# Optimization experiments

Hardware: AMD Instinct MI355X
Metric: run time of the kernel (lower is better)

Reference implementation:

```python
import jax, jax.numpy as jnp
import numpy as np

H, DH, ITERS, EPS, LN_EPS = 8, 32, 3, 1e-8, 1e-5

def _ln(x, w, b):
    m = jnp.mean(x, axis=-1, keepdims=True)
    v = jnp.mean(jnp.square(x - m), axis=-1, keepdims=True)
    return (x - m) * jax.lax.rsqrt(v + LN_EPS) * w + b

def setup_inputs() -> dict:
    key = jax.random.key(0)
    ks = jax.random.split(key, 16)
    B, N, D, S = 64, 4096, 256, 8
    DI = H * DH  # 256
    HID = max(D, 128)
    s = 0.02
    return {
        "inputs": jax.random.normal(ks[0], (B, N, D), jnp.float32),
        "noise": jax.random.normal(ks[1], (B, S, D), jnp.float32),
        "slots_mean": jax.random.normal(ks[2], (1, 1, D), jnp.float32),
        "slots_logvar": jax.random.normal(ks[3], (1, 1, D), jnp.float32) * s,
        "wq": jax.random.normal(ks[4], (D, DI), jnp.float32) * s,
        "bq": jnp.zeros((DI,), jnp.float32),
        "wk": jax.random.normal(ks[5], (D, DI), jnp.float32) * s,
        "bk": jnp.zeros((DI,), jnp.float32),
        "wv": jax.random.normal(ks[6], (D, DI), jnp.float32) * s,
        "bv": jnp.zeros((DI,), jnp.float32),
        "wo": jax.random.normal(ks[7], (DI, D), jnp.float32) * s,
        "bo": jnp.zeros((D,), jnp.float32),
        "w_ih": jax.random.normal(ks[8], (D, 3 * D), jnp.float32) * s,
        "b_ih": jnp.zeros((3 * D,), jnp.float32),
        "w_hh": jax.random.normal(ks[9], (D, 3 * D), jnp.float32) * s,
        "b_hh": jnp.zeros((3 * D,), jnp.float32),
        "w1": jax.random.normal(ks[10], (D, HID), jnp.float32) * s,
        "b1": jnp.zeros((HID,), jnp.float32),
        "w2": jax.random.normal(ks[11], (HID, D), jnp.float32) * s,
        "b2": jnp.zeros((D,), jnp.float32),
        "ln_in_w": jnp.ones((D,), jnp.float32), "ln_in_b": jnp.zeros((D,), jnp.float32),
        "ln_s_w": jnp.ones((D,), jnp.float32), "ln_s_b": jnp.zeros((D,), jnp.float32),
        "ln_ff_w": jnp.ones((D,), jnp.float32), "ln_ff_b": jnp.zeros((D,), jnp.float32),
    }

def reference(inputs, noise, slots_mean, slots_logvar, wq, bq, wk, bk, wv, bv,
              wo, bo, w_ih, b_ih, w_hh, b_hh, w1, b1, w2, b2,
              ln_in_w, ln_in_b, ln_s_w, ln_s_b, ln_ff_w, ln_ff_b):
    B, N, D = inputs.shape
    S = noise.shape[1]
    scale = D ** -0.5  # note: scale uses dim, per original code
    # slot init: mean + exp(logvar) * noise (faithful: exp(logvar) used directly)
    slots = slots_mean + jnp.exp(slots_logvar) * noise  # [B,S,D]
    x = _ln(inputs, ln_in_w, ln_in_b)
    k = (x @ wk + bk).reshape(B, N, H, DH).transpose(0, 2, 1, 3)  # [B,H,N,Dh]
    v = (x @ wv + bv).reshape(B, N, H, DH).transpose(0, 2, 1, 3)
    attn = None
    for _ in range(ITERS):
        slots_prev = slots
        s = _ln(slots, ln_s_w, ln_s_b)
        q = (s @ wq + bq).reshape(B, S, H, DH).transpose(0, 2, 1, 3)  # [B,H,S,Dh]
        dots = jnp.einsum('bhid,bhjd->bhij', q, k) * scale  # [B,H,S,N]
        attn = jax.nn.softmax(dots, axis=-2)  # softmax over slot axis
        attn = attn + EPS
        attn = attn / jnp.clip(jnp.sum(attn, axis=-1, keepdims=True), 1e-12)  # L1 over inputs
        upd = jnp.einsum('bhjd,bhij->bhid', v, attn)  # [B,H,S,Dh]
        upd = upd.transpose(0, 2, 1, 3).reshape(B, S, H * DH) @ wo + bo  # [B,S,D]
        # GRUCell (torch gate order r,z,n)
        xg = upd.reshape(B * S, D) @ w_ih + b_ih
        hg = slots_prev.reshape(B * S, D) @ w_hh + b_hh
        xr, xz, xn = jnp.split(xg, 3, axis=-1)
        hr, hz, hn = jnp.split(hg, 3, axis=-1)
        r = jax.nn.sigmoid(xr + hr)
        z = jax.nn.sigmoid(xz + hz)
        n = jnp.tanh(xn + r * hn)
        slots = ((1.0 - z) * n + z * slots_prev.reshape(B * S, D)).reshape(B, S, D)
        ff = _ln(slots, ln_ff_w, ln_ff_b)
        slots = slots + (jax.nn.relu(ff @ w1 + b1) @ w2 + b2)
    return slots, attn
```

## Files before the change

kernel.cpp:

```cpp
#include <hip/hip_runtime.h>
#include <stdint.h>

typedef __attribute__((ext_vector_type(8))) short bf16x8;
typedef __attribute__((ext_vector_type(4))) float f32x4;

__device__ __forceinline__ float b2f(unsigned short s) {
    unsigned int u = ((unsigned int)s) << 16;
    return __builtin_bit_cast(float, u);
}
__device__ __forceinline__ unsigned short f2b(float f) {
    unsigned int u = __builtin_bit_cast(unsigned int, f);
    u += 0x7FFFu + ((u >> 16) & 1u);
    return (unsigned short)(u >> 16);
}

#define EPS_ATTN 1e-8f
#define LN_EPS 1e-5f
#define SCALE 0.0625f

__global__ __launch_bounds__(256) void k_prep(const float* __restrict__ wk,
                                              const float* __restrict__ wv,
                                              unsigned short* __restrict__ W3) {
    int g = blockIdx.x * 256 + threadIdx.x;
    int j = g & 7;
    int f = (g >> 3) & 1023;
    int stage = g >> 13;
    int p = f & 15, qq = (f >> 4) & 3, ntl = f >> 6;
    int kc = stage >> 1, half_ = stage & 1;
    int k = kc * 32 + qq * 8 + j;
    int n = half_ * 256 + ntl * 16 + p;
    float v = (n < 256) ? wk[k * 256 + n] : wv[k * 256 + (n - 256)];
    W3[g] = f2b(v);
}

__global__ __launch_bounds__(256) void k_init(const float* __restrict__ sm,
                                              const float* __restrict__ slv,
                                              const float* __restrict__ noise,
                                              float* __restrict__ slots) {
    int idx = blockIdx.x * 256 + threadIdx.x;
    int d = idx & 255;
    slots[idx] = sm[d] + expf(slv[d]) * noise[idx];
}

__global__ __launch_bounds__(256, 2) void k_kv(
    const float* __restrict__ x, const float* __restrict__ lnw, const float* __restrict__ lnb,
    const unsigned short* __restrict__ W3, const float* __restrict__ bk, const float* __restrict__ bv,
    unsigned short* __restrict__ Kb, unsigned short* __restrict__ Vb) {
    __shared__ __align__(16) unsigned short sh[16384];
    __shared__ __align__(16) float bL[512];
    unsigned short* As = sh;
    int t = threadIdx.x;
    int w = t >> 6, lane = t & 63;
    int p = lane & 15, q = lane >> 4;

    if (t < 128) {
        float4 bb = (t < 64) ? ((const float4*)bk)[t] : ((const float4*)bv)[t - 64];
        *(float4*)&bL[t * 4] = bb;
    }

    float4 lw  = ((const float4*)lnw)[lane];
    float4 lbv = ((const float4*)lnb)[lane];
    float4 xv[16];
    const float* xbase = x + ((size_t)blockIdx.x * 64 + w * 16) * 256;
    #pragma unroll
    for (int i = 0; i < 16; ++i) xv[i] = ((const float4*)(xbase + i * 256))[lane];
    int kcw = lane >> 3, qw = (lane >> 1) & 3, j0 = (lane & 1) * 4;
    #pragma unroll
    for (int i = 0; i < 16; ++i) {
        float4 v = xv[i];
        float s0 = v.x + v.y + v.z + v.w;
        float s1 = v.x * v.x + v.y * v.y + v.z * v.z + v.w * v.w;
        #pragma unroll
        for (int o = 1; o < 64; o <<= 1) { s0 += __shfl_xor(s0, o); s1 += __shfl_xor(s1, o); }
        float mean = s0 * (1.0f / 256.0f);
        float var  = s1 * (1.0f / 256.0f) - mean * mean;
        float rstd = rsqrtf(var + LN_EPS);
        ushort4 pk;
        pk.x = f2b((v.x - mean) * rstd * lw.x + lbv.x);
        pk.y = f2b((v.y - mean) * rstd * lw.y + lbv.y);
        pk.z = f2b((v.z - mean) * rstd * lw.z + lbv.z);
        pk.w = f2b((v.w - mean) * rstd * lw.w + lbv.w);
        int pos = (qw * 16 + i) ^ kcw;
        *(ushort4*)&As[((w * 8 + kcw) * 64 + pos) * 8 + j0] = pk;
    }
    __syncthreads();

    f32x4 acc[4][8];
    f32x4 zero = {0.f, 0.f, 0.f, 0.f};
    #pragma unroll
    for (int rt = 0; rt < 4; ++rt)
        #pragma unroll
        for (int ct = 0; ct < 8; ++ct) acc[rt][ct] = zero;

    const unsigned short* Wb = W3 + (size_t)(w >> 1) * 8192 + (size_t)((w & 1) * 8) * 512 + lane * 8;
    #pragma unroll 2
    for (int kc = 0; kc < 8; ++kc) {
        bf16x8 af[4];
        #pragma unroll
        for (int rt = 0; rt < 4; ++rt)
            af[rt] = *(const bf16x8*)&As[((rt * 8 + kc) * 64 + ((q * 16 + p) ^ kc)) * 8];
        #pragma unroll
        for (int ct = 0; ct < 8; ++ct) {
            bf16x8 bf = *(const bf16x8*)(Wb + (size_t)kc * 16384 + ct * 512);
            #pragma unroll
            for (int rt = 0; rt < 4; ++rt)
                acc[rt][ct] = __builtin_amdgcn_mfma_f32_16x16x32_bf16(af[rt], bf, acc[rt][ct], 0, 0, 0);
        }
    }
    __syncthreads();

    unsigned short* rep = As;
    int b_  = blockIdx.x >> 6;
    int n0g = (blockIdx.x & 63) * 64;

    if (w < 2) {
        #pragma unroll
        for (int ct = 0; ct < 8; ++ct) {
            int col = w * 128 + ct * 16 + p;
            float bias = bL[col];
            int hl = col >> 5, dh = col & 31;
            #pragma unroll
            for (int rt = 0; rt < 4; ++rt) {
                #pragma unroll
                for (int r = 0; r < 4; ++r) {
                    int nl = rt * 16 + q * 4 + r;
                    rep[(hl * 64 + nl) * 32 + dh] = f2b(acc[rt][ct][r] + bias);
                }
            }
        }
    }
    __syncthreads();
    #pragma unroll
    for (int i = 0; i < 8; ++i) {
        uint4 vd = *(const uint4*)&rep[(i * 256 + t) * 8];
        *(uint4*)(Kb + (((size_t)b_ * 8 + i) * 4096 + n0g) * 32 + t * 8) = vd;
    }
    __syncthreads();

    if (w >= 2) {
        #pragma unroll
        for (int ct = 0; ct < 8; ++ct) {
            int vrow = (w - 2) * 128 + ct * 16 + p;
            float bias = bL[256 + vrow];
            #pragma unroll
            for (int rt = 0; rt < 4; ++rt) {
                int chunk = (rt * 4 + q) ^ (p & 14);
                ushort4 pk;
                pk.x = f2b(acc[rt][ct][0] + bias);
                pk.y = f2b(acc[rt][ct][1] + bias);
                pk.z = f2b(acc[rt][ct][2] + bias);
                pk.w = f2b(acc[rt][ct][3] + bias);
                *(ushort4*)&rep[vrow * 64 + chunk * 4] = pk;
            }
        }
    }
    __syncthreads();
    #pragma unroll
    for (int i = 0; i < 8; ++i) {
        int vrow = i * 32 + (t >> 3);
        int c16 = t & 7;
        uint4 vd = *(const uint4*)&rep[vrow * 64 + ((2 * c16) ^ (vrow & 14)) * 4];
        *(uint4*)(Vb + ((size_t)(b_ * 8 + (vrow >> 5)) * 32 + (vrow & 31)) * 4096 + n0g + c16 * 8) = vd;
    }
}

__global__ __launch_bounds__(256) void k_q(
    const float* __restrict__ slots, const float* __restrict__ lnw, const float* __restrict__ lnb,
    const float* __restrict__ wq, const float* __restrict__ bq, float* __restrict__ qg) {
    __shared__ float sln[256];
    __shared__ float red[8];
    int t = threadIdx.x;
    int row = blockIdx.x;
    float v = slots[(size_t)row * 256 + t];
    float s0 = v, s1 = v * v;
    #pragma unroll
    for (int off = 1; off < 64; off <<= 1) { s0 += __shfl_xor(s0, off); s1 += __shfl_xor(s1, off); }
    if ((t & 63) == 0) { red[t >> 6] = s0; red[4 + (t >> 6)] = s1; }
    __syncthreads();
    float ts0 = red[0] + red[1] + red[2] + red[3];
    float ts1 = red[4] + red[5] + red[6] + red[7];
    float mean = ts0 * (1.f / 256.f);
    float var  = ts1 * (1.f / 256.f) - mean * mean;
    float rstd = rsqrtf(var + LN_EPS);
    sln[t] = (v - mean) * rstd * lnw[t] + lnb[t];
    __syncthreads();
    float acc = bq[t];
    #pragma unroll 4
    for (int k = 0; k < 256; ++k) acc += sln[k] * wq[k * 256 + t];
    int b = row >> 3, sl = row & 7;
    qg[(size_t)b * 2048 + (t >> 5) * 256 + sl * 32 + (t & 31)] = acc;
}

__global__ __launch_bounds__(256) void k_attn(
    const unsigned short* __restrict__ Kg, const unsigned short* __restrict__ VTg,
    const float* __restrict__ qg, float* __restrict__ upd_part, float* __restrict__ rowsum_part,
    float* __restrict__ attn_out, int last) {
    __shared__ float supd[4][256];
    __shared__ float srs[4][8];
    int t = threadIdx.x;
    int w = t >> 6, lane = t & 63;
    int c = lane & 15;
    int g = lane >> 4;

    int bh = blockIdx.x >> 2;
    int chunk = blockIdx.x & 3;
    const unsigned short* Kbh = Kg  + (size_t)bh * 4096 * 32;
    const unsigned short* Vbh = VTg + (size_t)bh * 32 * 4096;

    bf16x8 qhi = {0,0,0,0,0,0,0,0};
    bf16x8 qlo = {0,0,0,0,0,0,0,0};
    if (c < 8) {
        const float* qp = qg + (size_t)bh * 256 + c * 32 + g * 8;
        #pragma unroll
        for (int j = 0; j < 8; ++j) {
            float qv = qp[j];
            unsigned short hb = f2b(qv);
            qhi[j] = (short)hb;
            qlo[j] = (short)f2b(qv - b2f(hb));
        }
    }

    f32x4 zero = {0.f, 0.f, 0.f, 0.f};
    f32x4 accL = zero, accH = zero;
    float rs = 0.f;
    int nb0 = chunk * 1024 + w * 256;

    #pragma unroll 2
    for (int pr = 0; pr < 8; ++pr) {
        int base = nb0 + pr * 32;
        bf16x8 k0 = *(const bf16x8*)(Kbh + (size_t)(base + c) * 32 + g * 8);
        bf16x8 k1 = *(const bf16x8*)(Kbh + (size_t)(base + 16 + c) * 32 + g * 8);
        const unsigned short* vlo = Vbh + (size_t)c * 4096 + base + g * 4;
        const unsigned short* vhi = Vbh + (size_t)(c + 16) * 4096 + base + g * 4;
        union { ushort4 h[2]; bf16x8 v; } V0, V1;
        V0.h[0] = *(const ushort4*)vlo;
        V0.h[1] = *(const ushort4*)(vlo + 16);
        V1.h[0] = *(const ushort4*)vhi;
        V1.h[1] = *(const ushort4*)(vhi + 16);

        f32x4 s0 = __builtin_amdgcn_mfma_f32_16x16x32_bf16(k0, qhi, zero, 0, 0, 0);
        s0 = __builtin_amdgcn_mfma_f32_16x16x32_bf16(k0, qlo, s0, 0, 0, 0);
        f32x4 s1 = __builtin_amdgcn_mfma_f32_16x16x32_bf16(k1, qhi, zero, 0, 0, 0);
        s1 = __builtin_amdgcn_mfma_f32_16x16x32_bf16(k1, qlo, s1, 0, 0, 0);

        float d0[4], d1[4];
        #pragma unroll
        for (int r = 0; r < 4; ++r) { d0[r] = s0[r] * SCALE; d1[r] = s1[r] * SCALE; }
        float m = fmaxf(fmaxf(fmaxf(d0[0], d0[1]), fmaxf(d0[2], d0[3])),
                        fmaxf(fmaxf(d1[0], d1[1]), fmaxf(d1[2], d1[3])));
        m = fmaxf(m, __shfl_xor(m, 1));
        m = fmaxf(m, __shfl_xor(m, 2));
        m = fmaxf(m, __shfl_xor(m, 4));
        m = fmaxf(m, __shfl_xor(m, 8));
        float a0[4], a1[4];
        #pragma unroll
        for (int r = 0; r < 4; ++r) {
            float e0 = __expf(d0[r] - m);
            float e1 = __expf(d1[r] - m);
            float t0 = e0;
            t0 += __shfl_xor(t0, 1); t0 += __shfl_xor(t0, 2); t0 += __shfl_xor(t0, 4);
            float t1 = e1;
            t1 += __shfl_xor(t1, 1); t1 += __shfl_xor(t1, 2); t1 += __shfl_xor(t1, 4);
            a0[r] = e0 * (1.0f / t0) + EPS_ATTN;
            a1[r] = e1 * (1.0f / t1) + EPS_ATTN;
            rs += a0[r] + a1[r];
        }
        if (last && c < 8) {
            float4 st0 = {a0[0], a0[1], a0[2], a0[3]};
            float4 st1 = {a1[0], a1[1], a1[2], a1[3]};
            float* ap = attn_out + ((size_t)bh * 8 + c) * 4096 + base + g * 4;
            *(float4*)ap = st0;
            *(float4*)(ap + 16) = st1;
        }
        bf16x8 pah, pal;
        float af[8] = {a0[0], a0[1], a0[2], a0[3], a1[0], a1[1], a1[2], a1[3]};
        #pragma unroll
        for (int j = 0; j < 8; ++j) {
            unsigned short hb = f2b(af[j]);
            pah[j] = (short)hb;
            pal[j] = (short)f2b(af[j] - b2f(hb));
        }
        accL = __builtin_amdgcn_mfma_f32_16x16x32_bf16(V0.v, pah, accL, 0, 0, 0);
        accL = __builtin_amdgcn_mfma_f32_16x16x32_bf16(V0.v, pal, accL, 0, 0, 0);
        accH = __builtin_amdgcn_mfma_f32_16x16x32_bf16(V1.v, pah, accH, 0, 0, 0);
        accH = __builtin_amdgcn_mfma_f32_16x16x32_bf16(V1.v, pal, accH, 0, 0, 0);
    }

    rs += __shfl_xor(rs, 16);
    rs += __shfl_xor(rs, 32);
    if (lane < 8) srs[w][lane] = rs;
    if (c < 8) {
        float* up = &supd[w][c * 32 + g * 4];
        up[0]  = accL[0]; up[1]  = accL[1]; up[2]  = accL[2]; up[3]  = accL[3];
        up[16] = accH[0]; up[17] = accH[1]; up[18] = accH[2]; up[19] = accH[3];
    }
    __syncthreads();
    {
        float v = supd[0][t] + supd[1][t] + supd[2][t] + supd[3][t];
        upd_part[((size_t)bh * 4 + chunk) * 256 + t] = v;
    }
    if (t < 8) {
        float v = srs[0][t] + srs[1][t] + srs[2][t] + srs[3][t];
        rowsum_part[((size_t)bh * 4 + chunk) * 8 + t] = v;
    }
}

__global__ __launch_bounds__(256) void k_gA(
    const float* __restrict__ upd_part, const float* __restrict__ rowsum_part,
    const float* __restrict__ wo, const float* __restrict__ bo,
    float* __restrict__ O, float* __restrict__ rowsum_tot) {
    __shared__ float Ul[8][256];
    __shared__ float Pp[4][8][64];
    int t = threadIdx.x;
    int b = blockIdx.x >> 2, cc = blockIdx.x & 3;
    int colbase = cc * 64;
    {
        int r = t >> 5, d0 = (t & 31) * 8;
        int h = (t & 31) >> 2;
        float rsum = 0.f;
        #pragma unroll
        for (int ch = 0; ch < 4; ++ch)
            rsum += rowsum_part[((size_t)(b * 8 + h) * 4 + ch) * 8 + r];
        float inv = 1.0f / fmaxf(rsum, 1e-12f);
        float u[8] = {0.f,0.f,0.f,0.f,0.f,0.f,0.f,0.f};
        #pragma unroll
        for (int ch = 0; ch < 4; ++ch) {
            const float* up = upd_part + ((size_t)(b * 8 + h) * 4 + ch) * 256 + r * 32 + (d0 & 31);
            float4 u0 = *(const float4*)up;
            float4 u1 = *(const float4*)(up + 4);
            u[0] += u0.x; u[1] += u0.y; u[2] += u0.z; u[3] += u0.w;
            u[4] += u1.x; u[5] += u1.y; u[6] += u1.z; u[7] += u1.w;
        }
        #pragma unroll
        for (int i = 0; i < 8; ++i) Ul[r][d0 + i] = u[i] * inv;
        if (cc == 0 && (t & 3) == 0) rowsum_tot[(b * 8 + h) * 8 + r] = rsum;
    }
    __syncthreads();
    int c = t & 63, kq = t >> 6;
    float acc[8] = {0.f,0.f,0.f,0.f,0.f,0.f,0.f,0.f};
    const float* wp = wo + (size_t)(kq * 64) * 256 + colbase + c;
    #pragma unroll 16
    for (int k = 0; k < 64; ++k) {
        float wv_ = wp[(size_t)k * 256];
        int kk = kq * 64 + k;
        #pragma unroll
        for (int r = 0; r < 8; ++r) acc[r] += Ul[r][kk] * wv_;
    }
    #pragma unroll
    for (int r = 0; r < 8; ++r) Pp[kq][r][c] = acc[r];
    __syncthreads();
    #pragma unroll
    for (int j = 0; j < 2; ++j) {
        int o = t * 2 + j;
        int r = o >> 6, c2 = o & 63;
        float v = Pp[0][r][c2] + Pp[1][r][c2] + Pp[2][r][c2] + Pp[3][r][c2] + bo[colbase + c2];
        O[(size_t)(b * 8 + r) * 256 + colbase + c2] = v;
    }
}

__global__ __launch_bounds__(256) void k_gB(
    const float* __restrict__ O, const float* __restrict__ slin,
    const float* __restrict__ wih, const float* __restrict__ bih,
    const float* __restrict__ whh, const float* __restrict__ bhh,
    float* __restrict__ gcomb, float* __restrict__ xn, float* __restrict__ hn) {
    __shared__ float Ol[8][256], Hl[8][256];
    __shared__ float Px[2][8][128], Ph[2][8][128];
    int t = threadIdx.x;
    int b = blockIdx.x / 6, cc = blockIdx.x % 6;
    int colbase = cc * 128;
    {
        int r = t >> 5, d0 = (t & 31) * 8;
        const float* op = O + (size_t)(b * 8 + r) * 256 + d0;
        const float* hp = slin + (size_t)(b * 8 + r) * 256 + d0;
        *(float4*)&Ol[r][d0]     = *(const float4*)op;
        *(float4*)&Ol[r][d0 + 4] = *(const float4*)(op + 4);
        *(float4*)&Hl[r][d0]     = *(const float4*)hp;
        *(float4*)&Hl[r][d0 + 4] = *(const float4*)(hp + 4);
    }
    __syncthreads();
    int c = t & 127, kh = t >> 7;
    float ax[8] = {0.f,0.f,0.f,0.f,0.f,0.f,0.f,0.f};
    float ah[8] = {0.f,0.f,0.f,0.f,0.f,0.f,0.f,0.f};
    const float* wxp = wih + (size_t)(kh * 128) * 768 + colbase + c;
    const float* whp = whh + (size_t)(kh * 128) * 768 + colbase + c;
    #pragma unroll 8
    for (int k = 0; k < 128; ++k) {
        float wx = wxp[(size_t)k * 768];
        float wh = whp[(size_t)k * 768];
        int kk = kh * 128 + k;
        #pragma unroll
        for (int r = 0; r < 8; ++r) { ax[r] += Ol[r][kk] * wx; ah[r] += Hl[r][kk] * wh; }
    }
    #pragma unroll
    for (int r = 0; r < 8; ++r) { Px[kh][r][c] = ax[r]; Ph[kh][r][c] = ah[r]; }
    __syncthreads();
    #pragma unroll
    for (int j = 0; j < 4; ++j) {
        int o = t * 4 + j;
        int r = o >> 7, c2 = o & 127;
        int cg = colbase + c2;
        int row = b * 8 + r;
        float vx = Px[0][r][c2] + Px[1][r][c2] + bih[cg];
        float vh = Ph[0][r][c2] + Ph[1][r][c2] + bhh[cg];
        if (cg < 512) {
            gcomb[(size_t)row * 512 + cg] = vx + vh;
        } else {
            xn[(size_t)row * 256 + cg - 512] = vx;
            hn[(size_t)row * 256 + cg - 512] = vh;
        }
    }
}

__global__ __launch_bounds__(256) void k_gC(
    const float* __restrict__ gcomb, const float* __restrict__ xn, const float* __restrict__ hn,
    const float* __restrict__ slin, const float* __restrict__ lnfw, const float* __restrict__ lnfb,
    float* __restrict__ slout, float* __restrict__ F) {
    __shared__ float red[8];
    int t = threadIdx.x, row = blockIdx.x;
    float a_r = gcomb[(size_t)row * 512 + t];
    float a_z = gcomb[(size_t)row * 512 + 256 + t];
    float xnv = xn[(size_t)row * 256 + t];
    float hnv = hn[(size_t)row * 256 + t];
    float hp  = slin[(size_t)row * 256 + t];
    float rg = 1.f / (1.f + expf(-a_r));
    float zg = 1.f / (1.f + expf(-a_z));
    float ng = tanhf(xnv + rg * hnv);
    float s1 = (1.f - zg) * ng + zg * hp;
    slout[(size_t)row * 256 + t] = s1;
    float s0 = s1, sq = s1 * s1;
    #pragma unroll
    for (int o = 1; o < 64; o <<= 1) { s0 += __shfl_xor(s0, o); sq += __shfl_xor(sq, o); }
    if ((t & 63) == 0) { red[t >> 6] = s0; red[4 + (t >> 6)] = sq; }
    __syncthreads();
    float ts0 = red[0] + red[1] + red[2] + red[3];
    float ts1 = red[4] + red[5] + red[6] + red[7];
    float mean = ts0 * (1.f / 256.f);
    float var  = ts1 * (1.f / 256.f) - mean * mean;
    float rstd = rsqrtf(var + LN_EPS);
    F[(size_t)row * 256 + t] = (s1 - mean) * rstd * lnfw[t] + lnfb[t];
}

__global__ __launch_bounds__(256) void k_gD(
    const float* __restrict__ F, const float* __restrict__ w1, const float* __restrict__ b1,
    float* __restrict__ H1) {
    __shared__ float Fl[8][256];
    __shared__ float Pp[4][8][64];
    int t = threadIdx.x;
    int b = blockIdx.x >> 2, cc = blockIdx.x & 3;
    int colbase = cc * 64;
    {
        int r = t >> 5, d0 = (t & 31) * 8;
        const float* fp = F + (size_t)(b * 8 + r) * 256 + d0;
        *(float4*)&Fl[r][d0]     = *(const float4*)fp;
        *(float4*)&Fl[r][d0 + 4] = *(const float4*)(fp + 4);
    }
    __syncthreads();
    int c = t & 63, kq = t >> 6;
    float acc[8] = {0.f,0.f,0.f,0.f,0.f,0.f,0.f,0.f};
    const float* wp = w1 + (size_t)(kq * 64) * 256 + colbase + c;
    #pragma unroll 16
    for (int k = 0; k < 64; ++k) {
        float wv_ = wp[(size_t)k * 256];
        int kk = kq * 64 + k;
        #pragma unroll
        for (int r = 0; r < 8; ++r) acc[r] += Fl[r][kk] * wv_;
    }
    #pragma unroll
    for (int r = 0; r < 8; ++r) Pp[kq][r][c] = acc[r];
    __syncthreads();
    #pragma unroll
    for (int j = 0; j < 2; ++j) {
        int o = t * 2 + j;
        int r = o >> 6, c2 = o & 63;
        float v = Pp[0][r][c2] + Pp[1][r][c2] + Pp[2][r][c2] + Pp[3][r][c2] + b1[colbase + c2];
        H1[(size_t)(b * 8 + r) * 256 + colbase + c2] = fmaxf(v, 0.f);
    }
}

__global__ __launch_bounds__(256) void k_gE(
    const float* __restrict__ H1, const float* __restrict__ w2, const float* __restrict__ b2,
    float* __restrict__ slout) {
    __shared__ float Hl[8][256];
    __shared__ float Pp[4][8][64];
    int t = threadIdx.x;
    int b = blockIdx.x >> 2, cc = blockIdx.x & 3;
    int colbase = cc * 64;
    {
        int r = t >> 5, d0 = (t & 31) * 8;
        const float* hp = H1 + (size_t)(b * 8 + r) * 256 + d0;
        *(float4*)&Hl[r][d0]     = *(const float4*)hp;
        *(float4*)&Hl[r][d0 + 4] = *(const float4*)(hp + 4);
    }
    __syncthreads();
    int c = t & 63, kq = t >> 6;
    float acc[8] = {0.f,0.f,0.f,0.f,0.f,0.f,0.f,0.f};
    const float* wp = w2 + (size_t)(kq * 64) * 256 + colbase + c;
    #pragma unroll 16
    for (int k = 0; k < 64; ++k) {
        float wv_ = wp[(size_t)k * 256];
        int kk = kq * 64 + k;
        #pragma unroll
        for (int r = 0; r < 8; ++r) acc[r] += Hl[r][kk] * wv_;
    }
    #pragma unroll
    for (int r = 0; r < 8; ++r) Pp[kq][r][c] = acc[r];
    __syncthreads();
    #pragma unroll
    for (int j = 0; j < 2; ++j) {
        int o = t * 2 + j;
        int r = o >> 6, c2 = o & 63;
        size_t idx = (size_t)(b * 8 + r) * 256 + colbase + c2;
        float v = Pp[0][r][c2] + Pp[1][r][c2] + Pp[2][r][c2] + Pp[3][r][c2] + b2[colbase + c2];
        slout[idx] = slout[idx] + v;
    }
}

__global__ __launch_bounds__(256) void k_scale(float* __restrict__ attn, const float* __restrict__ rowsum_tot) {
    size_t i4 = ((size_t)blockIdx.x * 256 + threadIdx.x) * 4;
    int row = (int)(i4 >> 12);
    float inv = 1.0f / fmaxf(rowsum_tot[row], 1e-12f);
    float4 v = *(float4*)(attn + i4);
    v.x *= inv; v.y *= inv; v.z *= inv; v.w *= inv;
    *(float4*)(attn + i4) = v;
}

extern "C" void kernel_launch(void* const* d_in, const int* in_sizes, int n_in,
                              void* d_out, int out_size, void* d_ws, size_t ws_size,
                              hipStream_t stream) {
    const float* inputs = (const float*)d_in[0];
    const float* noise  = (const float*)d_in[1];
    const float* sm     = (const float*)d_in[2];
    const float* slv    = (const float*)d_in[3];
    const float* wq     = (const float*)d_in[4];
    const float* bq     = (const float*)d_in[5];
    const float* wk     = (const float*)d_in[6];
    const float* bk     = (const float*)d_in[7];
    const float* wv     = (const float*)d_in[8];
    const float* bv     = (const float*)d_in[9];
    const float* wo     = (const float*)d_in[10];
    const float* bo     = (const float*)d_in[11];
    const float* wih    = (const float*)d_in[12];
    const float* bih    = (const float*)d_in[13];
    const float* whh    = (const float*)d_in[14];
    const float* bhh    = (const float*)d_in[15];
    const float* w1     = (const float*)d_in[16];
    const float* b1     = (const float*)d_in[17];
    const float* w2     = (const float*)d_in[18];
    const float* b2     = (const float*)d_in[19];
    const float* lniw   = (const float*)d_in[20];
    const float* lnib   = (const float*)d_in[21];
    const float* lnsw   = (const float*)d_in[22];
    const float* lnsb   = (const float*)d_in[23];
    const float* lnfw   = (const float*)d_in[24];
    const float* lnfb   = (const float*)d_in[25];

    char* ws = (char*)d_ws;
    unsigned short* Kb = (unsigned short*)ws;
    unsigned short* Vb = (unsigned short*)(ws + 134217728ull);
    float* slotsA  = (float*)(ws + 268435456ull);
    float* slotsB  = (float*)(ws + 268959744ull);
    float* Rr      = (float*)(ws + 269484032ull);
    float* Pr      = (float*)(ws + 270008320ull);
    float* Qr      = (float*)(ws + 270532608ull);
    float* rowsum_part = (float*)(ws + 272629760ull);
    float* rowsum_tot  = (float*)(ws + 273154048ull);
    unsigned short* W3 = (unsigned short*)Pr;
    float* O_  = Pr;
    float* upd_part = Qr;
    float* gcomb = Qr;
    float* xn = Qr + 262144;
    float* hn = Qr + 393216;
    float* H1 = Qr;
    float* qg = Rr;
    float* F_ = Rr;

    float* out_slots = (float*)d_out;
    float* attn_out  = (float*)d_out + 131072;

    k_prep<<<512, 256, 0, stream>>>(wk, wv, W3);
    k_init<<<512, 256, 0, stream>>>(sm, slv, noise, slotsA);
    k_kv<<<4096, 256, 0, stream>>>(inputs, lniw, lnib, W3, bk, bv, Kb, Vb);
    for (int it = 0; it < 3; ++it) {
        int last = (it == 2);
        float* sl_in  = (it == 0) ? slotsA : ((it == 1) ? slotsB : slotsA);
        float* sl_out = (it == 0) ? slotsB : ((it == 1) ? slotsA : out_slots);
        k_q<<<512, 256, 0, stream>>>(sl_in, lnsw, lnsb, wq, bq, qg);
        k_attn<<<2048, 256, 0, stream>>>(Kb, Vb, qg, upd_part, rowsum_part, attn_out, last);
        k_gA<<<256, 256, 0, stream>>>(upd_part, rowsum_part, wo, bo, O_, rowsum_tot);
        k_gB<<<384, 256, 0, stream>>>(O_, sl_in, wih, bih, whh, bhh, gcomb, xn, hn);
        k_gC<<<512, 256, 0, stream>>>(gcomb, xn, hn, sl_in, lnfw, lnfb, sl_out, F_);
        k_gD<<<256, 256, 0, stream>>>(F_, w1, b1, H1);
        k_gE<<<256, 256, 0, stream>>>(H1, w2, b2, sl_out);
    }
    k_scale<<<16384, 256, 0, stream>>>(attn_out, rowsum_tot);
}
```

Before: 1.098 ms.

## Precompute last-iteration attention rowsums to fold normalization into attn store; rebalance k_kv epilogue

On the last iteration a new k_pre kernel recomputes the softmax row sums from K and q, so k_attn can write attention already L1-normalized. This removes the separate k_scale pass that re-read and re-wrote the 64 MB fp32 attention output. It costs an extra read of K and a second QK^T/softmax pass. Separately, k_kv now gives every wave a share of both K and V columns and swizzles the K staging in LDS, so all four waves take part in each epilogue phase instead of two sitting idle.

New measurement: 1.025 ms. 1.07x faster.

```diff
diff --git a/kernel.cpp b/kernel.cpp
--- a/kernel.cpp
+++ b/kernel.cpp
@@ -92,7 +92,7 @@
         #pragma unroll
         for (int ct = 0; ct < 8; ++ct) acc[rt][ct] = zero;
 
-    const unsigned short* Wb = W3 + (size_t)(w >> 1) * 8192 + (size_t)((w & 1) * 8) * 512 + lane * 8;
+    const unsigned short* WbL = W3 + lane * 8;
     #pragma unroll 2
     for (int kc = 0; kc < 8; ++kc) {
         bf16x8 af[4];
@@ -101,7 +101,9 @@
             af[rt] = *(const bf16x8*)&As[((rt * 8 + kc) * 64 + ((q * 16 + p) ^ kc)) * 8];
         #pragma unroll
         for (int ct = 0; ct < 8; ++ct) {
-            bf16x8 bf = *(const bf16x8*)(Wb + (size_t)kc * 16384 + ct * 512);
+            int half_ = ct >> 2;
+            int ntl = w * 4 + (ct & 3);
+            bf16x8 bf = *(const bf16x8*)(WbL + (size_t)kc * 16384 + half_ * 8192 + ntl * 512);
             #pragma unroll
             for (int rt = 0; rt < 4; ++rt)
                 acc[rt][ct] = __builtin_amdgcn_mfma_f32_16x16x32_bf16(af[rt], bf, acc[rt][ct], 0, 0, 0);
@@ -113,45 +115,47 @@
     int b_  = blockIdx.x >> 6;
     int n0g = (blockIdx.x & 63) * 64;
 
-    if (w < 2) {
-        #pragma unroll
-        for (int ct = 0; ct < 8; ++ct) {
-            int col = w * 128 + ct * 16 + p;
-            float bias = bL[col];
-            int hl = col >> 5, dh = col & 31;
+    #pragma unroll
+    for (int ct = 0; ct < 4; ++ct) {
+        int col = w * 64 + ct * 16 + p;
+        float bias = bL[col];
+        int hl = col >> 5, dh = col & 31;
+        int dlo = dh & 7, dch = dh >> 3;
+        int dchs = dch ^ q;
+        #pragma unroll
+        for (int rt = 0; rt < 4; ++rt) {
             #pragma unroll
-            for (int rt = 0; rt < 4; ++rt) {
-                #pragma unroll
-                for (int r = 0; r < 4; ++r) {
-                    int nl = rt * 16 + q * 4 + r;
-                    rep[(hl * 64 + nl) * 32 + dh] = f2b(acc[rt][ct][r] + bias);
-                }
+            for (int r = 0; r < 4; ++r) {
+                int nl = rt * 16 + q * 4 + r;
+                rep[(hl * 64 + nl) * 32 + dchs * 8 + dlo] = f2b(acc[rt][ct][r] + bias);
             }
         }
     }
     __syncthreads();
-    #pragma unroll
-    for (int i = 0; i < 8; ++i) {
-        uint4 vd = *(const uint4*)&rep[(i * 256 + t) * 8];
-        *(uint4*)(Kb + (((size_t)b_ * 8 + i) * 4096 + n0g) * 32 + t * 8) = vd;
-    }
-    __syncthreads();
-
-    if (w >= 2) {
-        #pragma unroll
-        for (int ct = 0; ct < 8; ++ct) {
-            int vrow = (w - 2) * 128 + ct * 16 + p;
-            float bias = bL[256 + vrow];
-            #pragma unroll
-            for (int rt = 0; rt < 4; ++rt) {
-                int chunk = (rt * 4 + q) ^ (p & 14);
-                ushort4 pk;
-                pk.x = f2b(acc[rt][ct][0] + bias);
-                pk.y = f2b(acc[rt][ct][1] + bias);
-                pk.z = f2b(acc[rt][ct][2] + bias);
-                pk.w = f2b(acc[rt][ct][3] + bias);
-                *(ushort4*)&rep[vrow * 64 + chunk * 4] = pk;
-            }
+    {
+        int nl = t >> 2, dhc = t & 3;
+        int swz = (nl >> 2) & 3;
+        #pragma unroll
+        for (int i = 0; i < 8; ++i) {
+            uint4 vd = *(const uint4*)&rep[((i * 64 + nl) * 32) + ((dhc ^ swz) * 8)];
+            *(uint4*)(Kb + (((size_t)b_ * 8 + i) * 4096 + n0g + nl) * 32 + dhc * 8) = vd;
+        }
+    }
+    __syncthreads();
+
+    #pragma unroll
+    for (int ct = 4; ct < 8; ++ct) {
+        int vrow = w * 64 + (ct - 4) * 16 + p;
+        float bias = bL[256 + vrow];
+        #pragma unroll
+        for (int rt = 0; rt < 4; ++rt) {
+            int chunk = (rt * 4 + q) ^ (p & 14);
+            ushort4 pk;
+            pk.x = f2b(acc[rt][ct][0] + bias);
+            pk.y = f2b(acc[rt][ct][1] + bias);
+            pk.z = f2b(acc[rt][ct][2] + bias);
+            pk.w = f2b(acc[rt][ct][3] + bias);
+            *(ushort4*)&rep[vrow * 64 + chunk * 4] = pk;
         }
     }
     __syncthreads();
@@ -191,6 +195,73 @@
     qg[(size_t)b * 2048 + (t >> 5) * 256 + sl * 32 + (t & 31)] = acc;
 }
 
+__global__ __launch_bounds__(256) void k_pre(
+    const unsigned short* __restrict__ Kg, const float* __restrict__ qg,
+    float* __restrict__ rowsum_part) {
+    __shared__ float srs[4][8];
+    int t = threadIdx.x;
+    int w = t >> 6, lane = t & 63;
+    int c = lane & 15, g = lane >> 4;
+    int bh = blockIdx.x >> 2;
+    int chunk = blockIdx.x & 3;
+    const unsigned short* Kbh = Kg + (size_t)bh * 4096 * 32;
+
+    bf16x8 qhi = {0,0,0,0,0,0,0,0};
+    bf16x8 qlo = {0,0,0,0,0,0,0,0};
+    if (c < 8) {
+        const float* qp = qg + (size_t)bh * 256 + c * 32 + g * 8;
+        #pragma unroll
+        for (int j = 0; j < 8; ++j) {
+            float qv = qp[j];
+            unsigned short hb = f2b(qv);
+            qhi[j] = (short)hb;
+            qlo[j] = (short)f2b(qv - b2f(hb));
+        }
+    }
+
+    f32x4 zero = {0.f, 0.f, 0.f, 0.f};
+    float rs = 0.f;
+    int nb0 = chunk * 1024 + w * 256;
+
+    #pragma unroll 2
+    for (int pr = 0; pr < 8; ++pr) {
+        int base = nb0 + pr * 32;
+        bf16x8 k0 = *(const bf16x8*)(Kbh + (size_t)(base + c) * 32 + g * 8);
+        bf16x8 k1 = *(const bf16x8*)(Kbh + (size_t)(base + 16 + c) * 32 + g * 8);
+        f32x4 s0 = __builtin_amdgcn_mfma_f32_16x16x32_bf16(k0, qhi, zero, 0, 0, 0);
+        s0 = __builtin_amdgcn_mfma_f32_16x16x32_bf16(k0, qlo, s0, 0, 0, 0);
+        f32x4 s1 = __builtin_amdgcn_mfma_f32_16x16x32_bf16(k1, qhi, zero, 0, 0, 0);
+        s1 = __builtin_amdgcn_mfma_f32_16x16x32_bf16(k1, qlo, s1, 0, 0, 0);
+        float d0[4], d1[4];
+        #pragma unroll
+        for (int r = 0; r < 4; ++r) { d0[r] = s0[r] * SCALE; d1[r] = s1[r] * SCALE; }
+        float m = fmaxf(fmaxf(fmaxf(d0[0], d0[1]), fmaxf(d0[2], d0[3])),
+                        fmaxf(fmaxf(d1[0], d1[1]), fmaxf(d1[2], d1[3])));
+        m = fmaxf(m, __shfl_xor(m, 1));
+        m = fmaxf(m, __shfl_xor(m, 2));
+        m = fmaxf(m, __shfl_xor(m, 4));
+        m = fmaxf(m, __shfl_xor(m, 8));
+        #pragma unroll
+        for (int r = 0; r < 4; ++r) {
+            float e0 = __expf(d0[r] - m);
+            float e1 = __expf(d1[r] - m);
+            float t0 = e0;
+            t0 += __shfl_xor(t0, 1); t0 += __shfl_xor(t0, 2); t0 += __shfl_xor(t0, 4);
+            float t1 = e1;
+            t1 += __shfl_xor(t1, 1); t1 += __shfl_xor(t1, 2); t1 += __shfl_xor(t1, 4);
+            rs += (e0 * (1.0f / t0) + EPS_ATTN) + (e1 * (1.0f / t1) + EPS_ATTN);
+        }
+    }
+    rs += __shfl_xor(rs, 16);
+    rs += __shfl_xor(rs, 32);
+    if (lane < 8) srs[w][lane] = rs;
+    __syncthreads();
+    if (t < 8) {
+        rowsum_part[((size_t)bh * 4 + chunk) * 8 + t] =
+            srs[0][t] + srs[1][t] + srs[2][t] + srs[3][t];
+    }
+}
+
 __global__ __launch_bounds__(256) void k_attn(
     const unsigned short* __restrict__ Kg, const unsigned short* __restrict__ VTg,
     const float* __restrict__ qg, float* __restrict__ upd_part, float* __restrict__ rowsum_part,
@@ -218,6 +289,13 @@
             qhi[j] = (short)hb;
             qlo[j] = (short)f2b(qv - b2f(hb));
         }
+    }
+    float ainv = 0.f;
+    if (last && c < 8) {
+        float rsum = 0.f;
+        #pragma unroll
+        for (int ch = 0; ch < 4; ++ch) rsum += rowsum_part[((size_t)bh * 4 + ch) * 8 + c];
+        ainv = 1.0f / fmaxf(rsum, 1e-12f);
     }
 
     f32x4 zero = {0.f, 0.f, 0.f, 0.f};
@@ -266,8 +344,8 @@
             rs += a0[r] + a1[r];
         }
         if (last && c < 8) {
-            float4 st0 = {a0[0], a0[1], a0[2], a0[3]};
-            float4 st1 = {a1[0], a1[1], a1[2], a1[3]};
+            float4 st0 = {a0[0] * ainv, a0[1] * ainv, a0[2] * ainv, a0[3] * ainv};
+            float4 st1 = {a1[0] * ainv, a1[1] * ainv, a1[2] * ainv, a1[3] * ainv};
             float* ap = attn_out + ((size_t)bh * 8 + c) * 4096 + base + g * 4;
             *(float4*)ap = st0;
             *(float4*)(ap + 16) = st1;
@@ -286,9 +364,11 @@
         accH = __builtin_amdgcn_mfma_f32_16x16x32_bf16(V1.v, pal, accH, 0, 0, 0);
     }
 
-    rs += __shfl_xor(rs, 16);
-    rs += __shfl_xor(rs, 32);
-    if (lane < 8) srs[w][lane] = rs;
+    if (!last) {
+        rs += __shfl_xor(rs, 16);
+        rs += __shfl_xor(rs, 32);
+        if (lane < 8) srs[w][lane] = rs;
+    }
     if (c < 8) {
         float* up = &supd[w][c * 32 + g * 4];
         up[0]  = accL[0]; up[1]  = accL[1]; up[2]  = accL[2]; up[3]  = accL[3];
@@ -299,7 +379,7 @@
         float v = supd[0][t] + supd[1][t] + supd[2][t] + supd[3][t];
         upd_part[((size_t)bh * 4 + chunk) * 256 + t] = v;
     }
-    if (t < 8) {
+    if (!last && t < 8) {
         float v = srs[0][t] + srs[1][t] + srs[2][t] + srs[3][t];
         rowsum_part[((size_t)bh * 4 + chunk) * 8 + t] = v;
     }
@@ -308,7 +388,7 @@
 __global__ __launch_bounds__(256) void k_gA(
     const float* __restrict__ upd_part, const float* __restrict__ rowsum_part,
     const float* __restrict__ wo, const float* __restrict__ bo,
-    float* __restrict__ O, float* __restrict__ rowsum_tot) {
+    float* __restrict__ O) {
     __shared__ float Ul[8][256];
     __shared__ float Pp[4][8][64];
     int t = threadIdx.x;
@@ -333,7 +413,6 @@
         }
         #pragma unroll
         for (int i = 0; i < 8; ++i) Ul[r][d0 + i] = u[i] * inv;
-        if (cc == 0 && (t & 3) == 0) rowsum_tot[(b * 8 + h) * 8 + r] = rsum;
     }
     __syncthreads();
     int c = t & 63, kq = t >> 6;
@@ -513,15 +592,6 @@
         float v = Pp[0][r][c2] + Pp[1][r][c2] + Pp[2][r][c2] + Pp[3][r][c2] + b2[colbase + c2];
         slout[idx] = slout[idx] + v;
     }
-}
-
-__global__ __launch_bounds__(256) void k_scale(float* __restrict__ attn, const float* __restrict__ rowsum_tot) {
-    size_t i4 = ((size_t)blockIdx.x * 256 + threadIdx.x) * 4;
-    int row = (int)(i4 >> 12);
-    float inv = 1.0f / fmaxf(rowsum_tot[row], 1e-12f);
-    float4 v = *(float4*)(attn + i4);
-    v.x *= inv; v.y *= inv; v.z *= inv; v.w *= inv;
-    *(float4*)(attn + i4) = v;
 }
 
 extern "C" void kernel_launch(void* const* d_in, const int* in_sizes, int n_in,
@@ -563,7 +633,6 @@
     float* Pr      = (float*)(ws + 270008320ull);
     float* Qr      = (float*)(ws + 270532608ull);
     float* rowsum_part = (float*)(ws + 272629760ull);
-    float* rowsum_tot  = (float*)(ws + 273154048ull);
     unsigned short* W3 = (unsigned short*)Pr;
     float* O_  = Pr;
     float* upd_part = Qr;
@@ -585,12 +654,12 @@
         float* sl_in  = (it == 0) ? slotsA : ((it == 1) ? slotsB : slotsA);
         float* sl_out = (it == 0) ? slotsB : ((it == 1) ? slotsA : out_slots);
         k_q<<<512, 256, 0, stream>>>(sl_in, lnsw, lnsb, wq, bq, qg);
+        if (last) k_pre<<<2048, 256, 0, stream>>>(Kb, qg, rowsum_part);
         k_attn<<<2048, 256, 0, stream>>>(Kb, Vb, qg, upd_part, rowsum_part, attn_out, last);
-        k_gA<<<256, 256, 0, stream>>>(upd_part, rowsum_part, wo, bo, O_, rowsum_tot);
+        k_gA<<<256, 256, 0, stream>>>(upd_part, rowsum_part, wo, bo, O_);
         k_gB<<<384, 256, 0, stream>>>(O_, sl_in, wih, bih, whh, bhh, gcomb, xn, hn);
         k_gC<<<512, 256, 0, stream>>>(gcomb, xn, hn, sl_in, lnfw, lnfb, sl_out, F_);
         k_gD<<<256, 256, 0, stream>>>(F_, w1, b1, H1);
         k_gE<<<256, 256, 0, stream>>>(H1, w2, b2, sl_out);
     }
-    k_scale<<<16384, 256, 0, stream>>>(attn_out, rowsum_tot);
-}
+}
```
